# Optimization experiments

Hardware: AMD Instinct MI355X
Metric: run time of the kernel (lower is better)

## Reference

```python
import jax, jax.numpy as jnp
import numpy as np

B, S, E, H, L = 32, 1024, 768, 64, 2  # batch, seq (<=1024 per bias buffer), embed, head hidden, labels
MASKED_BIAS = jnp.float32(-10000.0)


def setup_inputs() -> dict:
    key = jax.random.key(0)
    ks = jax.random.split(key, 12)
    s = 0.02  # init scale
    return {
        "hidden": jax.random.normal(ks[0], (B, S, E), dtype=jnp.float32),
        "attention_mask": jnp.ones((B, S), dtype=jnp.float32),
        # torch nn.Linear weights are [out, in]
        "Wk": jax.random.normal(ks[1], (E, E), dtype=jnp.float32) * s,
        "bk": jnp.zeros((E,), dtype=jnp.float32),
        "Wq": jax.random.normal(ks[2], (E, E), dtype=jnp.float32) * s,
        "bq": jnp.zeros((E,), dtype=jnp.float32),
        "Wv": jax.random.normal(ks[3], (E, E), dtype=jnp.float32) * s,
        "bv": jnp.zeros((E,), dtype=jnp.float32),
        "W1": jax.random.normal(ks[4], (H, E), dtype=jnp.float32) * s,
        "b1": jnp.zeros((H,), dtype=jnp.float32),
        "W2": jax.random.normal(ks[5], (L, H), dtype=jnp.float32) * s,
        "b2": jnp.zeros((L,), dtype=jnp.float32),
    }


def reference(hidden, attention_mask, Wk, bk, Wq, bq, Wv, bv, W1, b1, W2, b2):
    # Single-head causal attention, NO 1/sqrt(d) scaling (faithful to source).
    # Dropout layers run in eval mode -> identity.
    seq = hidden.shape[1]
    q = hidden @ Wq.T + bq            # [B,S,E]
    k = hidden @ Wk.T + bk            # [B,S,E]
    v = hidden @ Wv.T + bv            # [B,S,E] (v_drop is identity in eval)
    w = jnp.einsum('bqe,bke->bqk', q, k)  # [B,S,S]
    causal = jnp.tril(jnp.ones((seq, seq), dtype=bool))  # bias[:, ns-nd:ns, :ns] with nd==ns
    w = jnp.where(causal, w, MASKED_BIAS.astype(w.dtype))
    am = (1.0 - attention_mask)[:, None, :] * -10000.0    # [B,1,S]
    w = jax.nn.softmax(w + am, axis=-1)
    h = jnp.einsum('bqk,bke->bqe', w, v)  # [B,S,E]
    h = jax.nn.relu(h @ W1.T + b1)        # [B,S,64]
    return h @ W2.T + b2                  # [B,S,L]
```

## Files before the change

kernel.cpp:

```cpp
#include <hip/hip_runtime.h>
#include <hip/hip_bf16.h>
#include <cstdio>


typedef _Float16 f16;
typedef f16    f16x8 __attribute__((ext_vector_type(8)));
typedef f16    f16x4 __attribute__((ext_vector_type(4)));
typedef __bf16 bfx8  __attribute__((ext_vector_type(8)));
typedef float  f32x4 __attribute__((ext_vector_type(4)));

#define MFMA_F16(a,b,c)  __builtin_amdgcn_mfma_f32_16x16x32_f16((a),(b),(c),0,0,0)
#define MFMA_BF16(a,b,c) __builtin_amdgcn_mfma_f32_16x16x32_bf16((a),(b),(c),0,0,0)

static constexpr int LDT2 = 264;

__device__ __forceinline__ void gl_lds16(const void* g, void* l) {
    __builtin_amdgcn_global_load_lds(
        (const __attribute__((address_space(1))) void*)g,
        (__attribute__((address_space(3))) void*)l, 16, 0, 0);
}

#define S_BARRIER()  asm volatile("s_barrier" ::: "memory")

__global__ __launch_bounds__(256) void cvt_all(
    const float* __restrict__ hidden,
    const float* __restrict__ Wq, const float* __restrict__ Wk, const float* __restrict__ Wv,
    f16* __restrict__ h16, f16* __restrict__ oq, f16* __restrict__ ok, f16* __restrict__ ov)
{
    const int bid = blockIdx.x;
    const float* src;
    f16* dst;
    int base;
    if (bid < 24576) {
        src = hidden; dst = h16;
        base = (bid * 256 + threadIdx.x) * 4;
    } else {
        int wz = (bid - 24576) / 576, wb = (bid - 24576) % 576;
        src = (wz == 0) ? Wq : (wz == 1) ? Wk : Wv;
        dst = (wz == 0) ? oq : (wz == 1) ? ok : ov;
        base = (wb * 256 + threadIdx.x) * 4;
    }
    f32x4 v = *(const f32x4*)(src + base);
    f16x4 o;
    #pragma unroll
    for (int e = 0; e < 4; ++e) o[e] = (f16)v[e];
    *(f16x4*)(dst + base) = o;
}

#define QPHASE(fr0, STAGE_STMT, GATE_STMT)                                        \
    {                                                                             \
        f16x8 afr[2][2];                                                          \
        _Pragma("unroll")                                                         \
        for (int i = 0; i < 2; ++i) {                                             \
            _Pragma("unroll")                                                     \
            for (int kk = 0; kk < 2; ++kk)                                        \
                afr[i][kk] = *(const f16x8*)&SA[kk * 8192 + (wr8 + (fr0) + i) * 512 + lq]; \
        }                                                                         \
        STAGE_STMT;                                                               \
        GATE_STMT;                                                                \
        S_BARRIER();                                                              \
        __builtin_amdgcn_s_setprio(1);                                            \
        _Pragma("unroll")                                                         \
        for (int i = 0; i < 2; ++i) {                                             \
            _Pragma("unroll")                                                     \
            for (int jj = 0; jj < 4; ++jj) {                                      \
                acc[(fr0) + i][jj] = MFMA_F16(afr[i][0], bfr[jj][0], acc[(fr0) + i][jj]); \
                acc[(fr0) + i][jj] = MFMA_F16(afr[i][1], bfr[jj][1], acc[(fr0) + i][jj]); \
            }                                                                     \
        }                                                                         \
        __builtin_amdgcn_s_setprio(0);                                            \
        S_BARRIER();                                                              \
    }

__global__ __launch_bounds__(512, 2) void qkv_kernel(
    const f16* __restrict__ h16,
    const f16* __restrict__ wq, const f16* __restrict__ wk, const f16* __restrict__ wv,
    const float* __restrict__ bq, const float* __restrict__ bk, const float* __restrict__ bv,
    f16* __restrict__ q16, f16* __restrict__ k16, __bf16* __restrict__ vT)
{
    const int f = blockIdx.x;
    const int xcd = f & 7;
    const int j = f >> 3;
    const int nt = j % 3;
    const int z  = (j / 3) % 3;
    const int mi = j / 9;
    const int mt = xcd + 8 * mi;
    const int m0 = mt * 256, n0 = nt * 256;

    const f16* W = (z == 0) ? wq : (z == 1) ? wk : wv;
    const float* bias = (z == 0) ? bq : (z == 1) ? bk : bv;

    __shared__ alignas(16) f16 S[65536];

    const int t = threadIdx.x, lane = t & 63, wave = t >> 6;
    const int wr = wave >> 2, wc = wave & 3;
    const int wr8 = wr * 8;
    const int quad = lane >> 4, l16 = lane & 15;
    const int lq = quad * 128 + l16 * 8;

    const f16* gA = h16 + (size_t)(m0 + l16) * 768 + quad * 8;
    const f16* gB = W   + (size_t)(n0 + l16) * 768 + quad * 8;
    int gofs[2], lofs[2];
    #pragma unroll
    for (int u = 0; u < 2; ++u) {
        int unit = wave * 2 + u;
        int kk = unit >> 3, c = unit & 7;
        gofs[u] = c * 16 * 768 + kk * 32;
        lofs[u] = kk * 8192 + c * 512;
    }
    auto stage = [&](int kt, int mat, int half) {
        const f16* gp = (mat ? gB : gA) + half * (128 * 768) + kt * 64;
        f16* lp = &S[(kt & 1) * 32768 + mat * 16384 + half * 4096];
        gl_lds16(gp + gofs[0], lp + lofs[0]);
        gl_lds16(gp + gofs[1], lp + lofs[1]);
    };

    f32x4 acc[8][4] = {};

    stage(0, 0, 0); stage(0, 0, 1); stage(0, 1, 0); stage(0, 1, 1);
    stage(1, 1, 0); stage(1, 1, 1);
    asm volatile("s_waitcnt vmcnt(4)" ::: "memory");
    S_BARRIER();

    f16x8 bfr[4][2];
    for (int kt = 0; kt < 12; ++kt) {
        const f16* SA = &S[(kt & 1) * 32768];
        const f16* SB = SA + 16384;
        #pragma unroll
        for (int jj = 0; jj < 4; ++jj) {
            #pragma unroll
            for (int kk = 0; kk < 2; ++kk)
                bfr[jj][kk] = *(const f16x8*)&SB[kk * 8192 + (wc * 4 + jj) * 512 + lq];
        }
        QPHASE(0, { if (kt + 1 < 12) stage(kt + 1, 0, 0); }, {});
        QPHASE(2, { if (kt + 1 < 12) stage(kt + 1, 0, 1); }, {});
        QPHASE(4, { if (kt + 2 < 12) stage(kt + 2, 1, 0); }, {});
        QPHASE(6, { if (kt + 2 < 12) stage(kt + 2, 1, 1); },
               {
                   if (kt + 2 < 12)       asm volatile("s_waitcnt vmcnt(4)" ::: "memory");
                   else if (kt + 1 < 12)  asm volatile("s_waitcnt vmcnt(0)" ::: "memory");
               });
    }

    if (z < 2) {
        f16* out = z ? k16 : q16;
        #pragma unroll
        for (int jj = 0; jj < 4; ++jj) {
            int col = n0 + wc * 64 + jj * 16 + l16;
            float bb = bias[col];
            #pragma unroll
            for (int fi = 0; fi < 8; ++fi) {
                #pragma unroll
                for (int r = 0; r < 4; ++r) {
                    int row = m0 + wr * 128 + fi * 16 + quad * 4 + r;
                    out[(size_t)row * 768 + col] = (f16)(acc[fi][jj][r] + bb);
                }
            }
        }
    } else {
        __bf16* Tb = (__bf16*)S;
        const int halfw = wc >> 1;
        const int bofs = (m0 >> 10) * 768;
        const int s0 = m0 & 1023;
        #pragma unroll
        for (int half = 0; half < 2; ++half) {
            __syncthreads();
            if (halfw == half) {
                #pragma unroll
                for (int jj = 0; jj < 4; ++jj) {
                    int el = (wc & 1) * 64 + jj * 16 + l16;
                    float bb = bias[n0 + half * 128 + el];
                    #pragma unroll
                    for (int fi = 0; fi < 8; ++fi) {
                        #pragma unroll
                        for (int r = 0; r < 4; ++r) {
                            int sl = wr * 128 + fi * 16 + quad * 4 + r;
                            Tb[el * LDT2 + sl] = (__bf16)(acc[fi][jj][r] + bb);
                        }
                    }
                }
            }
            __syncthreads();
            const int ch = (t & 31) * 8;
            const int rbase = t >> 5;
            #pragma unroll
            for (int p = 0; p < 8; ++p) {
                int e = rbase + p * 16;
                bfx8 val = *(const bfx8*)&Tb[e * LDT2 + ch];
                *(bfx8*)&vT[(size_t)(bofs + n0 + half * 128 + e) * 1024 + s0 + ch] = val;
            }
        }
    }
}

__global__ __launch_bounds__(256, 4) void logits_kernel(
    const f16* __restrict__ q16, const f16* __restrict__ k16,
    const float* __restrict__ amask, __bf16* __restrict__ pu, float* __restrict__ psum)
{
    const int f = blockIdx.x;
    const int xcd = f & 7;
    const int j = f >> 3;
    const int b = xcd + 8 * (j / 36);
    const int tile = j % 36;
    int mt = 0, base = 0;
    while (base + mt + 1 <= tile) { base += mt + 1; ++mt; }
    const int nt = tile - base;
    const int m0 = mt * 128, n0 = nt * 128;
    const size_t pb = (size_t)b << 20;
    const size_t qb = (size_t)b * 1024 * 768;

    __shared__ alignas(16) f16 S[2][8192];
    __shared__ float rs[2][128];

    const int t = threadIdx.x, lane = t & 63, wave = t >> 6;
    const int wm = (wave & 1) * 64, wn = (wave >> 1) * 64;
    const int quad = lane >> 4, l16 = lane & 15;

    const f16* gsrc[4];
    int ldst[4];
    #pragma unroll
    for (int u = 0; u < 4; ++u) {
        int c = wave * 4 + u;
        ldst[u] = c * 512;
        const f16* base2 = (c < 8) ? (q16 + qb + (size_t)(m0 + c * 16 + l16) * 768)
                                   : (k16 + qb + (size_t)(n0 + (c - 8) * 16 + l16) * 768);
        gsrc[u] = base2 + quad * 8;
    }

    f32x4 acc[4][4] = {};
    auto stage = [&](int k0, int buf) {
        #pragma unroll
        for (int u = 0; u < 4; ++u)
            gl_lds16(gsrc[u] + k0, &S[buf][ldst[u]]);
    };
    auto compute = [&](int buf) {
        f16x8 af[4], bg[4];
        #pragma unroll
        for (int i = 0; i < 4; ++i) {
            af[i] = *(const f16x8*)&S[buf][(wm / 16 + i) * 512 + quad * 128 + l16 * 8];
            bg[i] = *(const f16x8*)&S[buf][(8 + wn / 16 + i) * 512 + quad * 128 + l16 * 8];
        }
        #pragma unroll
        for (int i = 0; i < 4; ++i)
            #pragma unroll
            for (int jj = 0; jj < 4; ++jj)
                acc[i][jj] = MFMA_F16(af[i], bg[jj], acc[i][jj]);
    };

    stage(0, 0);
    int cur = 0;
    for (int k0 = 32; k0 < 768; k0 += 32) {
        __syncthreads();
        stage(k0, cur ^ 1);
        compute(cur);
        cur ^= 1;
    }
    __syncthreads();
    compute(cur);

    float rp[4][4] = {};
    #pragma unroll
    for (int jj = 0; jj < 4; ++jj) {
        int col = n0 + wn + jj * 16 + l16;
        float am = (1.0f - amask[b * 1024 + col]) * -10000.0f;
        #pragma unroll
        for (int i = 0; i < 4; ++i)
            #pragma unroll
            for (int r = 0; r < 4; ++r) {
                int row = m0 + wm + i * 16 + quad * 4 + r;
                float s = acc[i][jj][r] + am;
                float pval = (col <= row) ? __expf(fminf(s, 80.0f)) : 0.0f;
                pu[pb + (size_t)row * 1024 + col] = (__bf16)pval;
                rp[i][r] += pval;
            }
    }
    #pragma unroll
    for (int i = 0; i < 4; ++i)
        #pragma unroll
        for (int r = 0; r < 4; ++r) {
            float v = rp[i][r];
            v += __shfl_xor(v, 1, 64);
            v += __shfl_xor(v, 2, 64);
            v += __shfl_xor(v, 4, 64);
            v += __shfl_xor(v, 8, 64);
            if (l16 == 0) rs[wn >> 6][wm + i * 16 + quad * 4 + r] = v;
        }
    __syncthreads();
    if (t < 128)
        psum[((size_t)b * 1024 + m0 + t) * 8 + nt] = rs[0][t] + rs[1][t];
}

__global__ __launch_bounds__(256, 4) void pv_kernel(
    const __bf16* __restrict__ pu, const __bf16* __restrict__ vT,
    const float* __restrict__ psum, __bf16* __restrict__ h)
{
    const int f = blockIdx.x;
    const int xcd = f & 7;
    const int j = f >> 3;
    const int b = xcd + 8 * (j / 48);
    const int tile = j % 48;
    const int mt = 7 - tile / 6, nt = tile % 6;
    const int m0 = mt * 128, n0 = nt * 128;
    const size_t pb = (size_t)b << 20;
    const size_t vb = (size_t)b * 768 * 1024;

    __shared__ alignas(16) __bf16 S[2][8192];
    __shared__ float invl[128];

    const int t = threadIdx.x, lane = t & 63, wave = t >> 6;
    const int wm = (wave & 1) * 64, wn = (wave >> 1) * 64;
    const int quad = lane >> 4, l16 = lane & 15;

    if (t < 128) {
        int row = m0 + t;
        int lim = row >> 7;
        const float* pr = &psum[((size_t)b * 1024 + row) * 8];
        float s = 0.f;
        #pragma unroll
        for (int n = 0; n < 8; ++n) s += (n <= lim) ? pr[n] : 0.f;
        invl[t] = 1.0f / s;
    }

    const __bf16* gsrc[4];
    int ldst[4];
    #pragma unroll
    for (int u = 0; u < 4; ++u) {
        int c = wave * 4 + u;
        ldst[u] = c * 512;
        const __bf16* base = (c < 8) ? (pu + pb + (size_t)(m0 + c * 16 + l16) * 1024)
                                     : (vT + vb + (size_t)(n0 + (c - 8) * 16 + l16) * 1024);
        gsrc[u] = base + quad * 8;
    }

    f32x4 acc[4][4] = {};
    auto stage = [&](int k0, int buf) {
        #pragma unroll
        for (int u = 0; u < 4; ++u)
            gl_lds16(gsrc[u] + k0, &S[buf][ldst[u]]);
    };
    auto compute = [&](int buf) {
        bfx8 af[4], bg[4];
        #pragma unroll
        for (int i = 0; i < 4; ++i) {
            af[i] = *(const bfx8*)&S[buf][(wm / 16 + i) * 512 + quad * 128 + l16 * 8];
            bg[i] = *(const bfx8*)&S[buf][(8 + wn / 16 + i) * 512 + quad * 128 + l16 * 8];
        }
        #pragma unroll
        for (int i = 0; i < 4; ++i)
            #pragma unroll
            for (int jj = 0; jj < 4; ++jj)
                acc[i][jj] = MFMA_BF16(af[i], bg[jj], acc[i][jj]);
    };

    const int kend = m0 + 128;
    stage(0, 0);
    int cur = 0;
    for (int k0 = 32; k0 < kend; k0 += 32) {
        __syncthreads();
        stage(k0, cur ^ 1);
        compute(cur);
        cur ^= 1;
    }
    __syncthreads();
    compute(cur);

    #pragma unroll
    for (int jj = 0; jj < 4; ++jj) {
        int col = n0 + wn + jj * 16 + l16;
        #pragma unroll
        for (int i = 0; i < 4; ++i)
            #pragma unroll
            for (int r = 0; r < 4; ++r) {
                int rl = wm + i * 16 + quad * 4 + r;
                h[((size_t)b * 1024 + m0 + rl) * 768 + col] = (__bf16)(acc[i][jj][r] * invl[rl]);
            }
    }
}

__global__ __launch_bounds__(256) void mlp_kernel(
    const __bf16* __restrict__ h, const float* __restrict__ W1, const float* __restrict__ b1,
    const float* __restrict__ W2, const float* __restrict__ b2, float* __restrict__ out)
{
    const int wave = threadIdx.x >> 6, lane = threadIdx.x & 63;
    const int quad = lane >> 4, l16 = lane & 15;
    const int m0 = blockIdx.x * 64 + wave * 16;

    f32x4 acc[4] = {};
    for (int k0 = 0; k0 < 768; k0 += 32) {
        bfx8 af = *(const bfx8*)&h[(size_t)(m0 + l16) * 768 + k0 + quad * 8];
        #pragma unroll
        for (int jj = 0; jj < 4; ++jj) {
            const float* wp = W1 + (size_t)(jj * 16 + l16) * 768 + k0 + quad * 8;
            f32x4 w0 = *(const f32x4*)wp;
            f32x4 w1 = *(const f32x4*)(wp + 4);
            bfx8 bg;
            #pragma unroll
            for (int e = 0; e < 4; ++e) { bg[e] = (__bf16)w0[e]; bg[e + 4] = (__bf16)w1[e]; }
            acc[jj] = MFMA_BF16(af, bg, acc[jj]);
        }
    }
    float part[4][2] = {};
    #pragma unroll
    for (int jj = 0; jj < 4; ++jj) {
        int c = jj * 16 + l16;
        float bb = b1[c];
        float w20 = W2[c], w21 = W2[64 + c];
        #pragma unroll
        for (int r = 0; r < 4; ++r) {
            float x = fmaxf(acc[jj][r] + bb, 0.f);
            part[r][0] += x * w20;
            part[r][1] += x * w21;
        }
    }
    #pragma unroll
    for (int off = 1; off < 16; off <<= 1)
        #pragma unroll
        for (int r = 0; r < 4; ++r) {
            part[r][0] += __shfl_xor(part[r][0], off, 64);
            part[r][1] += __shfl_xor(part[r][1], off, 64);
        }
    if (l16 == 0) {
        #pragma unroll
        for (int r = 0; r < 4; ++r) {
            int row = m0 + quad * 4 + r;
            out[(size_t)row * 2 + 0] = part[r][0] + b2[0];
            out[(size_t)row * 2 + 1] = part[r][1] + b2[1];
        }
    }
}

extern "C" void kernel_launch(void* const* d_in, const int* in_sizes, int n_in,
                              void* d_out, int out_size, void* d_ws, size_t ws_size,
                              hipStream_t stream)
{
    const float* hidden = (const float*)d_in[0];
    const float* amask  = (const float*)d_in[1];
    const float* Wk = (const float*)d_in[2];
    const float* bk = (const float*)d_in[3];
    const float* Wq = (const float*)d_in[4];
    const float* bq = (const float*)d_in[5];
    const float* Wv = (const float*)d_in[6];
    const float* bv = (const float*)d_in[7];
    const float* W1 = (const float*)d_in[8];
    const float* b1 = (const float*)d_in[9];
    const float* W2 = (const float*)d_in[10];
    const float* b2 = (const float*)d_in[11];
    float* out = (float*)d_out;

    char* ws = (char*)d_ws;
    const size_t MB = 1024 * 1024;
    f16* h16 = (f16*)ws;
    f16* wq16 = (f16*)(ws + 48 * MB);
    f16* wk16 = wq16 + 589824;
    f16* wv16 = wk16 + 589824;
    __bf16* pu  = (__bf16*)ws;
    float*  psum = (float*)(ws + 64 * MB);
    f16* q16 = (f16*)(ws + 66 * MB);
    f16* k16 = (f16*)(ws + 114 * MB);
    __bf16* vT = (__bf16*)(ws + 162 * MB);
    __bf16* h  = (__bf16*)(ws + 66 * MB);
    const size_t NEED = 210 * MB;
    if (ws_size < NEED) {
        fprintf(stderr, "[Attn kernel] ws too small: %zu < %zu — skipping launches\n",
                ws_size, NEED);
        return;
    }

    cvt_all<<<24576 + 1728, 256, 0, stream>>>(
        hidden, Wq, Wk, Wv, h16, wq16, wk16, wv16);

    qkv_kernel<<<1152, 512, 0, stream>>>(
        h16, wq16, wk16, wv16, bq, bk, bv, q16, k16, vT);
    logits_kernel<<<1152, 256, 0, stream>>>(q16, k16, amask, pu, psum);
    pv_kernel<<<1536, 256, 0, stream>>>(pu, vT, psum, h);
    mlp_kernel<<<512, 256, 0, stream>>>(h, W1, b1, W2, b2, out);
}
```

Measured before the change: 519.7 us.

## Enlarge logits and PV tiles to 256x256 with QKV-style phased pipeline

Rewrites the logits and PV kernels to use 256x256 output tiles with 512-thread blocks, reusing the qkv kernel's four-phase schedule. That schedule stages data through global-to-LDS loads, uses explicit vmcnt waits and barriers, and raises priority around the MFMA blocks. Larger tiles cut redundant global loads of Q/K and P/V and raise MFMA density per block. In exchange the causal skip becomes coarser, so more masked work is computed. Grid size drops to 320/384 blocks, which risks lower occupancy and a wave-quantization tail on the GPU.

```diff
diff --git a/kernel.cpp b/kernel.cpp
--- a/kernel.cpp
+++ b/kernel.cpp
@@ -72,6 +72,31 @@
         S_BARRIER();                                                              \
     }
 
+#define QPHASE_BF(fr0, STAGE_STMT, GATE_STMT)                                     \
+    {                                                                             \
+        bfx8 afr[2][2];                                                           \
+        _Pragma("unroll")                                                         \
+        for (int i = 0; i < 2; ++i) {                                             \
+            _Pragma("unroll")                                                     \
+            for (int kk = 0; kk < 2; ++kk)                                        \
+                afr[i][kk] = *(const bfx8*)&SA[kk * 8192 + (wr8 + (fr0) + i) * 512 + lq]; \
+        }                                                                         \
+        STAGE_STMT;                                                               \
+        GATE_STMT;                                                                \
+        S_BARRIER();                                                              \
+        __builtin_amdgcn_s_setprio(1);                                            \
+        _Pragma("unroll")                                                         \
+        for (int i = 0; i < 2; ++i) {                                             \
+            _Pragma("unroll")                                                     \
+            for (int jj = 0; jj < 4; ++jj) {                                      \
+                acc[(fr0) + i][jj] = MFMA_BF16(afr[i][0], bfr[jj][0], acc[(fr0) + i][jj]); \
+                acc[(fr0) + i][jj] = MFMA_BF16(afr[i][1], bfr[jj][1], acc[(fr0) + i][jj]); \
+            }                                                                     \
+        }                                                                         \
+        __builtin_amdgcn_s_setprio(0);                                            \
+        S_BARRIER();                                                              \
+    }
+
 __global__ __launch_bounds__(512, 2) void qkv_kernel(
     const f16* __restrict__ h16,
     const f16* __restrict__ wq, const f16* __restrict__ wk, const f16* __restrict__ wv,
@@ -193,187 +218,201 @@
     }
 }
 
-__global__ __launch_bounds__(256, 4) void logits_kernel(
+__global__ __launch_bounds__(512, 2) void logits_kernel(
     const f16* __restrict__ q16, const f16* __restrict__ k16,
     const float* __restrict__ amask, __bf16* __restrict__ pu, float* __restrict__ psum)
 {
     const int f = blockIdx.x;
     const int xcd = f & 7;
     const int j = f >> 3;
-    const int b = xcd + 8 * (j / 36);
-    const int tile = j % 36;
-    int mt = 0, base = 0;
-    while (base + mt + 1 <= tile) { base += mt + 1; ++mt; }
-    const int nt = tile - base;
-    const int m0 = mt * 128, n0 = nt * 128;
+    const int b = xcd + 8 * (j / 10);
+    const int tile = j % 10;
+    int mt, nt;
+    if (tile < 4)      { mt = 3; nt = tile; }
+    else if (tile < 7) { mt = 2; nt = tile - 4; }
+    else if (tile < 9) { mt = 1; nt = tile - 7; }
+    else               { mt = 0; nt = 0; }
+    const int m0 = mt * 256, n0 = nt * 256;
     const size_t pb = (size_t)b << 20;
     const size_t qb = (size_t)b * 1024 * 768;
 
-    __shared__ alignas(16) f16 S[2][8192];
-    __shared__ float rs[2][128];
+    __shared__ alignas(16) f16 S[65536];
+    __shared__ float rs[4][256];
 
     const int t = threadIdx.x, lane = t & 63, wave = t >> 6;
-    const int wm = (wave & 1) * 64, wn = (wave >> 1) * 64;
+    const int wr = wave >> 2, wc = wave & 3;
+    const int wr8 = wr * 8;
     const int quad = lane >> 4, l16 = lane & 15;
-
-    const f16* gsrc[4];
-    int ldst[4];
-    #pragma unroll
-    for (int u = 0; u < 4; ++u) {
-        int c = wave * 4 + u;
-        ldst[u] = c * 512;
-        const f16* base2 = (c < 8) ? (q16 + qb + (size_t)(m0 + c * 16 + l16) * 768)
-                                   : (k16 + qb + (size_t)(n0 + (c - 8) * 16 + l16) * 768);
-        gsrc[u] = base2 + quad * 8;
-    }
-
-    f32x4 acc[4][4] = {};
-    auto stage = [&](int k0, int buf) {
-        #pragma unroll
-        for (int u = 0; u < 4; ++u)
-            gl_lds16(gsrc[u] + k0, &S[buf][ldst[u]]);
+    const int lq = quad * 128 + l16 * 8;
+
+    const f16* gA = q16 + qb + (size_t)(m0 + l16) * 768 + quad * 8;
+    const f16* gB = k16 + qb + (size_t)(n0 + l16) * 768 + quad * 8;
+    int gofs[2], lofs[2];
+    #pragma unroll
+    for (int u = 0; u < 2; ++u) {
+        int unit = wave * 2 + u;
+        int kk = unit >> 3, c = unit & 7;
+        gofs[u] = c * 16 * 768 + kk * 32;
+        lofs[u] = kk * 8192 + c * 512;
+    }
+    auto stage = [&](int kt, int mat, int half) {
+        const f16* gp = (mat ? gB : gA) + half * (128 * 768) + kt * 64;
+        f16* lp = &S[(kt & 1) * 32768 + mat * 16384 + half * 4096];
+        gl_lds16(gp + gofs[0], lp + lofs[0]);
+        gl_lds16(gp + gofs[1], lp + lofs[1]);
     };
-    auto compute = [&](int buf) {
-        f16x8 af[4], bg[4];
-        #pragma unroll
-        for (int i = 0; i < 4; ++i) {
-            af[i] = *(const f16x8*)&S[buf][(wm / 16 + i) * 512 + quad * 128 + l16 * 8];
-            bg[i] = *(const f16x8*)&S[buf][(8 + wn / 16 + i) * 512 + quad * 128 + l16 * 8];
-        }
-        #pragma unroll
-        for (int i = 0; i < 4; ++i)
-            #pragma unroll
-            for (int jj = 0; jj < 4; ++jj)
-                acc[i][jj] = MFMA_F16(af[i], bg[jj], acc[i][jj]);
-    };
-
-    stage(0, 0);
-    int cur = 0;
-    for (int k0 = 32; k0 < 768; k0 += 32) {
-        __syncthreads();
-        stage(k0, cur ^ 1);
-        compute(cur);
-        cur ^= 1;
-    }
-    __syncthreads();
-    compute(cur);
-
-    float rp[4][4] = {};
+
+    f32x4 acc[8][4] = {};
+
+    stage(0, 0, 0); stage(0, 0, 1); stage(0, 1, 0); stage(0, 1, 1);
+    stage(1, 1, 0); stage(1, 1, 1);
+    asm volatile("s_waitcnt vmcnt(4)" ::: "memory");
+    S_BARRIER();
+
+    f16x8 bfr[4][2];
+    for (int kt = 0; kt < 12; ++kt) {
+        const f16* SA = &S[(kt & 1) * 32768];
+        const f16* SB = SA + 16384;
+        #pragma unroll
+        for (int jj = 0; jj < 4; ++jj) {
+            #pragma unroll
+            for (int kk = 0; kk < 2; ++kk)
+                bfr[jj][kk] = *(const f16x8*)&SB[kk * 8192 + (wc * 4 + jj) * 512 + lq];
+        }
+        QPHASE(0, { if (kt + 1 < 12) stage(kt + 1, 0, 0); }, {});
+        QPHASE(2, { if (kt + 1 < 12) stage(kt + 1, 0, 1); }, {});
+        QPHASE(4, { if (kt + 2 < 12) stage(kt + 2, 1, 0); }, {});
+        QPHASE(6, { if (kt + 2 < 12) stage(kt + 2, 1, 1); },
+               {
+                   if (kt + 2 < 12)       asm volatile("s_waitcnt vmcnt(4)" ::: "memory");
+                   else if (kt + 1 < 12)  asm volatile("s_waitcnt vmcnt(0)" ::: "memory");
+               });
+    }
+
+    float rp[8][4] = {};
     #pragma unroll
     for (int jj = 0; jj < 4; ++jj) {
-        int col = n0 + wn + jj * 16 + l16;
+        int col = n0 + wc * 64 + jj * 16 + l16;
         float am = (1.0f - amask[b * 1024 + col]) * -10000.0f;
         #pragma unroll
-        for (int i = 0; i < 4; ++i)
+        for (int fi = 0; fi < 8; ++fi) {
             #pragma unroll
             for (int r = 0; r < 4; ++r) {
-                int row = m0 + wm + i * 16 + quad * 4 + r;
-                float s = acc[i][jj][r] + am;
+                int row = m0 + wr * 128 + fi * 16 + quad * 4 + r;
+                float s = acc[fi][jj][r] + am;
                 float pval = (col <= row) ? __expf(fminf(s, 80.0f)) : 0.0f;
                 pu[pb + (size_t)row * 1024 + col] = (__bf16)pval;
-                rp[i][r] += pval;
+                rp[fi][r] += pval;
             }
-    }
-    #pragma unroll
-    for (int i = 0; i < 4; ++i)
+        }
+    }
+    #pragma unroll
+    for (int fi = 0; fi < 8; ++fi) {
         #pragma unroll
         for (int r = 0; r < 4; ++r) {
-            float v = rp[i][r];
+            float v = rp[fi][r];
             v += __shfl_xor(v, 1, 64);
             v += __shfl_xor(v, 2, 64);
             v += __shfl_xor(v, 4, 64);
             v += __shfl_xor(v, 8, 64);
-            if (l16 == 0) rs[wn >> 6][wm + i * 16 + quad * 4 + r] = v;
-        }
+            if (l16 == 0) rs[wc][wr * 128 + fi * 16 + quad * 4 + r] = v;
+        }
+    }
     __syncthreads();
-    if (t < 128)
-        psum[((size_t)b * 1024 + m0 + t) * 8 + nt] = rs[0][t] + rs[1][t];
-}
-
-__global__ __launch_bounds__(256, 4) void pv_kernel(
+    if (t < 256)
+        psum[((size_t)b * 1024 + m0 + t) * 4 + nt] =
+            rs[0][t] + rs[1][t] + rs[2][t] + rs[3][t];
+}
+
+__global__ __launch_bounds__(512, 2) void pv_kernel(
     const __bf16* __restrict__ pu, const __bf16* __restrict__ vT,
     const float* __restrict__ psum, __bf16* __restrict__ h)
 {
     const int f = blockIdx.x;
     const int xcd = f & 7;
     const int j = f >> 3;
-    const int b = xcd + 8 * (j / 48);
-    const int tile = j % 48;
-    const int mt = 7 - tile / 6, nt = tile % 6;
-    const int m0 = mt * 128, n0 = nt * 128;
+    const int b = xcd + 8 * (j / 12);
+    const int tile = j % 12;
+    const int mt = 3 - tile / 3, nt = tile % 3;
+    const int m0 = mt * 256, n0 = nt * 256;
+    const int nkt = 4 * (mt + 1);
     const size_t pb = (size_t)b << 20;
     const size_t vb = (size_t)b * 768 * 1024;
 
-    __shared__ alignas(16) __bf16 S[2][8192];
-    __shared__ float invl[128];
+    __shared__ alignas(16) __bf16 S[65536];
+    __shared__ float invl[256];
 
     const int t = threadIdx.x, lane = t & 63, wave = t >> 6;
-    const int wm = (wave & 1) * 64, wn = (wave >> 1) * 64;
+    const int wr = wave >> 2, wc = wave & 3;
+    const int wr8 = wr * 8;
     const int quad = lane >> 4, l16 = lane & 15;
-
-    if (t < 128) {
+    const int lq = quad * 128 + l16 * 8;
+
+    if (t < 256) {
         int row = m0 + t;
-        int lim = row >> 7;
-        const float* pr = &psum[((size_t)b * 1024 + row) * 8];
+        int lim = row >> 8;
+        const float* pr = &psum[((size_t)b * 1024 + row) * 4];
         float s = 0.f;
         #pragma unroll
-        for (int n = 0; n < 8; ++n) s += (n <= lim) ? pr[n] : 0.f;
+        for (int n = 0; n < 4; ++n) s += (n <= lim) ? pr[n] : 0.f;
         invl[t] = 1.0f / s;
     }
 
-    const __bf16* gsrc[4];
-    int ldst[4];
-    #pragma unroll
-    for (int u = 0; u < 4; ++u) {
-        int c = wave * 4 + u;
-        ldst[u] = c * 512;
-        const __bf16* base = (c < 8) ? (pu + pb + (size_t)(m0 + c * 16 + l16) * 1024)
-                                     : (vT + vb + (size_t)(n0 + (c - 8) * 16 + l16) * 1024);
-        gsrc[u] = base + quad * 8;
-    }
-
-    f32x4 acc[4][4] = {};
-    auto stage = [&](int k0, int buf) {
-        #pragma unroll
-        for (int u = 0; u < 4; ++u)
-            gl_lds16(gsrc[u] + k0, &S[buf][ldst[u]]);
+    const __bf16* gA = pu + pb + (size_t)(m0 + l16) * 1024 + quad * 8;
+    const __bf16* gB = vT + vb + (size_t)(n0 + l16) * 1024 + quad * 8;
+    int gofs[2], lofs[2];
+    #pragma unroll
+    for (int u = 0; u < 2; ++u) {
+        int unit = wave * 2 + u;
+        int kk = unit >> 3, c = unit & 7;
+        gofs[u] = c * 16 * 1024 + kk * 32;
+        lofs[u] = kk * 8192 + c * 512;
+    }
+    auto stage = [&](int kt, int mat, int half) {
+        const __bf16* gp = (mat ? gB : gA) + half * (128 * 1024) + kt * 64;
+        __bf16* lp = &S[(kt & 1) * 32768 + mat * 16384 + half * 4096];
+        gl_lds16(gp + gofs[0], lp + lofs[0]);
+        gl_lds16(gp + gofs[1], lp + lofs[1]);
     };
-    auto compute = [&](int buf) {
-        bfx8 af[4], bg[4];
-        #pragma unroll
-        for (int i = 0; i < 4; ++i) {
-            af[i] = *(const bfx8*)&S[buf][(wm / 16 + i) * 512 + quad * 128 + l16 * 8];
-            bg[i] = *(const bfx8*)&S[buf][(8 + wn / 16 + i) * 512 + quad * 128 + l16 * 8];
-        }
-        #pragma unroll
-        for (int i = 0; i < 4; ++i)
-            #pragma unroll
-            for (int jj = 0; jj < 4; ++jj)
-                acc[i][jj] = MFMA_BF16(af[i], bg[jj], acc[i][jj]);
-    };
-
-    const int kend = m0 + 128;
-    stage(0, 0);
-    int cur = 0;
-    for (int k0 = 32; k0 < kend; k0 += 32) {
-        __syncthreads();
-        stage(k0, cur ^ 1);
-        compute(cur);
-        cur ^= 1;
-    }
-    __syncthreads();
-    compute(cur);
+
+    f32x4 acc[8][4] = {};
+
+    stage(0, 0, 0); stage(0, 0, 1); stage(0, 1, 0); stage(0, 1, 1);
+    stage(1, 1, 0); stage(1, 1, 1);
+    asm volatile("s_waitcnt vmcnt(4)" ::: "memory");
+    S_BARRIER();
+
+    bfx8 bfr[4][2];
+    for (int kt = 0; kt < nkt; ++kt) {
+        const __bf16* SA = &S[(kt & 1) * 32768];
+        const __bf16* SB = SA + 16384;
+        #pragma unroll
+        for (int jj = 0; jj < 4; ++jj) {
+            #pragma unroll
+            for (int kk = 0; kk < 2; ++kk)
+                bfr[jj][kk] = *(const bfx8*)&SB[kk * 8192 + (wc * 4 + jj) * 512 + lq];
+        }
+        QPHASE_BF(0, { if (kt + 1 < nkt) stage(kt + 1, 0, 0); }, {});
+        QPHASE_BF(2, { if (kt + 1 < nkt) stage(kt + 1, 0, 1); }, {});
+        QPHASE_BF(4, { if (kt + 2 < nkt) stage(kt + 2, 1, 0); }, {});
+        QPHASE_BF(6, { if (kt + 2 < nkt) stage(kt + 2, 1, 1); },
+               {
+                   if (kt + 2 < nkt)       asm volatile("s_waitcnt vmcnt(4)" ::: "memory");
+                   else if (kt + 1 < nkt)  asm volatile("s_waitcnt vmcnt(0)" ::: "memory");
+               });
+    }
 
     #pragma unroll
     for (int jj = 0; jj < 4; ++jj) {
-        int col = n0 + wn + jj * 16 + l16;
-        #pragma unroll
-        for (int i = 0; i < 4; ++i)
+        int col = n0 + wc * 64 + jj * 16 + l16;
+        #pragma unroll
+        for (int fi = 0; fi < 8; ++fi) {
             #pragma unroll
             for (int r = 0; r < 4; ++r) {
-                int rl = wm + i * 16 + quad * 4 + r;
-                h[((size_t)b * 1024 + m0 + rl) * 768 + col] = (__bf16)(acc[i][jj][r] * invl[rl]);
+                int rl = wr * 128 + fi * 16 + quad * 4 + r;
+                h[((size_t)b * 1024 + m0 + rl) * 768 + col] = (__bf16)(acc[fi][jj][r] * invl[rl]);
             }
+        }
     }
 }
 
@@ -471,7 +510,7 @@
 
     qkv_kernel<<<1152, 512, 0, stream>>>(
         h16, wq16, wk16, wv16, bq, bk, bv, q16, k16, vT);
-    logits_kernel<<<1152, 256, 0, stream>>>(q16, k16, amask, pu, psum);
-    pv_kernel<<<1536, 256, 0, stream>>>(pu, vT, psum, h);
+    logits_kernel<<<320, 512, 0, stream>>>(q16, k16, amask, pu, psum);
+    pv_kernel<<<384, 512, 0, stream>>>(pu, vT, psum, h);
     mlp_kernel<<<512, 256, 0, stream>>>(h, W1, b1, W2, b2, out);
 }
```

Result: no change. 516.6 us (-0.6%).
